# Performance work log

Hardware: AMD Instinct MI355X
Metric: run time of the kernel (lower is better)

The kernel has to match this reference:

```python
import jax, jax.numpy as jnp
import numpy as np

D_MODEL, D_STATE, D_CONV, EXPAND = 1024, 16, 4, 2
D_INNER = EXPAND * D_MODEL            # 2048
DT_RANK = (D_MODEL + 15) // 16        # 64
B, L = 2, 2048


def setup_inputs() -> dict:
    key = jax.random.key(0)
    ks = jax.random.split(key, 10)
    s = 0.02
    x = jax.random.normal(ks[0], (B, L, D_MODEL), dtype=jnp.float32)
    W_in = jax.random.normal(ks[1], (2 * D_INNER, D_MODEL), dtype=jnp.float32) * s
    conv_w = jax.random.normal(ks[2], (D_INNER, D_CONV), dtype=jnp.float32) * s
    conv_b = jnp.zeros((D_INNER,), dtype=jnp.float32)
    W_xproj = jax.random.normal(ks[3], (DT_RANK + 2 * D_STATE, D_INNER), dtype=jnp.float32) * s
    W_dtproj = jax.random.normal(ks[4], (D_INNER, DT_RANK), dtype=jnp.float32) * s
    dt_bias = jax.random.uniform(ks[5], (D_INNER,), dtype=jnp.float32, minval=-4.0, maxval=-2.0)
    # S4D-real init: A_log = log(1..d_state) per channel
    A_log = jnp.log(jnp.broadcast_to(jnp.arange(1, D_STATE + 1, dtype=jnp.float32), (D_INNER, D_STATE)))
    D = jnp.ones((D_INNER,), dtype=jnp.float32)
    W_out = jax.random.normal(ks[6], (D_MODEL, D_INNER), dtype=jnp.float32) * s
    return dict(x=x, W_in=W_in, conv_w=conv_w, conv_b=conv_b, W_xproj=W_xproj,
                W_dtproj=W_dtproj, dt_bias=dt_bias, A_log=A_log, D=D, W_out=W_out)


def _mamba_forward(x, W_in, conv_w, conv_b, W_xproj, W_dtproj, dt_bias, A_log, D, W_out):
    # in_proj: (B,L,d_model) -> (B,L,2*d_inner)
    xz = jnp.einsum('bld,ed->ble', x, W_in)
    u, z = jnp.split(xz, 2, axis=-1)                      # (B,L,Di) each
    # depthwise causal conv over time
    u_t = jnp.swapaxes(u, 1, 2)                           # (B,Di,L)
    u_c = jax.lax.conv_general_dilated(
        u_t, conv_w[:, None, :], window_strides=(1,), padding=[(D_CONV - 1, 0)],
        feature_group_count=D_INNER, dimension_numbers=('NCH', 'OIH', 'NCH'))
    u_c = jax.nn.silu(u_c + conv_b[None, :, None])
    u_c = jnp.swapaxes(u_c, 1, 2)                         # (B,L,Di)
    # x_proj -> dt, B_ssm, C_ssm
    x_dbl = jnp.einsum('bld,ed->ble', u_c, W_xproj)
    dt, B_ssm, C_ssm = jnp.split(x_dbl, [DT_RANK, DT_RANK + D_STATE], axis=-1)
    delta = jax.nn.softplus(jnp.einsum('blr,dr->bld', dt, W_dtproj) + dt_bias)  # (B,L,Di)
    A = -jnp.exp(A_log)                                   # (Di,Ds)

    def step(h, inp):
        d_t, b_t, c_t, u_t = inp                          # (B,Di),(B,Ds),(B,Ds),(B,Di)
        dA = jnp.exp(d_t[..., None] * A)                  # (B,Di,Ds)
        dBu = d_t[..., None] * b_t[:, None, :] * u_t[..., None]
        h = dA * h + dBu
        y = jnp.einsum('bds,bs->bd', h, c_t)
        return h, y

    h0 = jnp.zeros((B, D_INNER, D_STATE), dtype=x.dtype)
    xs = (jnp.swapaxes(delta, 0, 1), jnp.swapaxes(B_ssm, 0, 1),
          jnp.swapaxes(C_ssm, 0, 1), jnp.swapaxes(u_c, 0, 1))
    _, ys = jax.lax.scan(step, h0, xs)                    # (L,B,Di)
    y = jnp.swapaxes(ys, 0, 1) + u_c * D                  # skip term D*u
    y = y * jax.nn.silu(z)                                # gate
    return jnp.einsum('bld,ed->ble', y, W_out)            # (B,L,d_model)


def reference(x, W_in, conv_w, conv_b, W_xproj, W_dtproj, dt_bias, A_log, D, W_out):
    return _mamba_forward(x, W_in, conv_w, conv_b, W_xproj, W_dtproj, dt_bias, A_log, D, W_out)
```

## Files before the change

### kernel.cpp

```cpp
#include <hip/hip_runtime.h>
#include <cstdint>
#include <cstddef>

constexpr int Bc = 2, Lc = 2048, DM = 1024, DI = 2048, DS = 16, DR = 64, NX = 96;
constexpr int BL = Bc * Lc;
constexpr int NC = 32, CH = 64;
constexpr int BDS = Bc * DI * DS;
constexpr float LOG2E = 1.44269504f;

typedef __attribute__((ext_vector_type(8))) short bf16x8;
typedef __attribute__((ext_vector_type(4))) float f32x4;
typedef unsigned short u16;

__device__ __forceinline__ u16 f2b(float f) {
  uint32_t u = __float_as_uint(f);
  return (u16)((u + 0x7FFFu + ((u >> 16) & 1u)) >> 16);
}
__device__ __forceinline__ float b2f(u16 h) {
  return __uint_as_float(((uint32_t)h) << 16);
}

__global__ __launch_bounds__(256) void cvt_hilo(
    const float* __restrict__ in, u16* __restrict__ hi, u16* __restrict__ lo,
    int n4) {
  int i = blockIdx.x * 256 + threadIdx.x;
  if (i >= n4) return;
  float4 v = reinterpret_cast<const float4*>(in)[i];
  ushort4 H, L;
  H.x = f2b(v.x); L.x = f2b(v.x - b2f(H.x));
  H.y = f2b(v.y); L.y = f2b(v.y - b2f(H.y));
  H.z = f2b(v.z); L.z = f2b(v.z - b2f(H.z));
  H.w = f2b(v.w); L.w = f2b(v.w - b2f(H.w));
  reinterpret_cast<ushort4*>(hi)[i] = H;
  reinterpret_cast<ushort4*>(lo)[i] = L;
}

__global__ __launch_bounds__(256) void cvt_pad_wx(
    const float* __restrict__ w, u16* __restrict__ hi, u16* __restrict__ lo) {
  int i = blockIdx.x * 256 + threadIdx.x;
  int f = i * 4;
  int row = f >> 11;
  ushort4 H, L;
  H.x = H.y = H.z = H.w = 0; L = H;
  if (row < 96) {
    float4 v = *reinterpret_cast<const float4*>(&w[f]);
    H.x = f2b(v.x); L.x = f2b(v.x - b2f(H.x));
    H.y = f2b(v.y); L.y = f2b(v.y - b2f(H.y));
    H.z = f2b(v.z); L.z = f2b(v.z - b2f(H.z));
    H.w = f2b(v.w); L.w = f2b(v.w - b2f(H.w));
  }
  reinterpret_cast<ushort4*>(hi)[i] = H;
  reinterpret_cast<ushort4*>(lo)[i] = L;
}

__device__ __forceinline__ void stage_tile(
    const u16* __restrict__ g, u16* lds, int row0, int ld, int k0,
    int w, int lane) {
  #pragma unroll
  for (int i = 0; i < 2; ++i) {
    const int base = w * 1024 + i * 4096;
    const int o = base + lane * 16;
    const int row = o >> 6;
    const int sl = ((o >> 4) & 3) ^ ((row >> 1) & 3);
    const u16* src = g + (size_t)(row0 + row) * ld + (k0 + sl * 8);
    __builtin_amdgcn_global_load_lds(
        (const __attribute__((address_space(1))) unsigned int*)src,
        (__attribute__((address_space(3))) unsigned int*)(lds + base / 2),
        16, 0, 0);
  }
}

__device__ __forceinline__ void stage4(
    const u16* __restrict__ Ah, const u16* __restrict__ Al,
    const u16* __restrict__ Bh, const u16* __restrict__ Bl,
    u16* buf , int bm, int bn, int lda, int ldb,
    int k0, int w, int lane) {
  stage_tile(Ah, buf + 0 * 4096, bm, lda, k0, w, lane);
  stage_tile(Al, buf + 1 * 4096, bm, lda, k0, w, lane);
  stage_tile(Bh, buf + 2 * 4096, bn, ldb, k0, w, lane);
  stage_tile(Bl, buf + 3 * 4096, bn, ldb, k0, w, lane);
}

__device__ __forceinline__ bf16x8 ld_frag(const u16* plane, int rowbase, int lane) {
  const int row = rowbase + (lane & 15);
  const int kb = (lane >> 4) ^ ((row >> 1) & 3);
  return *reinterpret_cast<const bf16x8*>(
      reinterpret_cast<const char*>(plane) + row * 64 + kb * 16);
}

template<int EPI>
__global__ __launch_bounds__(256) void gemm_mfma(
    const u16* __restrict__ Ah, const u16* __restrict__ Al,
    const u16* __restrict__ Bh, const u16* __restrict__ Bl,
    const float* __restrict__ bias, float* __restrict__ C,
    int M, int N, int K, int lda, int ldb, int ldc) {
  __shared__ __align__(16) u16 lds[2][4][4096];
  const int tid = threadIdx.x;
  const int lane = tid & 63, w = tid >> 6;
  const int wr = w >> 1, wc = w & 1;
  const int bm = blockIdx.x * 128, bn = blockIdx.y * 128;

  f32x4 acc[4][4] = {};

  const int nt = K / 32;
  stage4(Ah, Al, Bh, Bl, &lds[0][0][0], bm, bn, lda, ldb, 0, w, lane);
  __syncthreads();

  int cur = 0;
  for (int t = 0; t < nt; ++t) {
    if (t + 1 < nt)
      stage4(Ah, Al, Bh, Bl, &lds[cur ^ 1][0][0], bm, bn, lda, ldb,
             (t + 1) * 32, w, lane);

    const u16* Lb = &lds[cur][0][0];
    bf16x8 ah[4], al[4], bh[4], bl[4];
    #pragma unroll
    for (int m = 0; m < 4; ++m) {
      ah[m] = ld_frag(Lb + 0 * 4096, wr * 64 + m * 16, lane);
      al[m] = ld_frag(Lb + 1 * 4096, wr * 64 + m * 16, lane);
    }
    #pragma unroll
    for (int n = 0; n < 4; ++n) {
      bh[n] = ld_frag(Lb + 2 * 4096, wc * 64 + n * 16, lane);
      bl[n] = ld_frag(Lb + 3 * 4096, wc * 64 + n * 16, lane);
    }
    __builtin_amdgcn_s_setprio(1);
    #pragma unroll
    for (int m = 0; m < 4; ++m)
      #pragma unroll
      for (int n = 0; n < 4; ++n)
        acc[m][n] = __builtin_amdgcn_mfma_f32_16x16x32_bf16(ah[m], bh[n], acc[m][n], 0, 0, 0);
    #pragma unroll
    for (int m = 0; m < 4; ++m)
      #pragma unroll
      for (int n = 0; n < 4; ++n)
        acc[m][n] = __builtin_amdgcn_mfma_f32_16x16x32_bf16(ah[m], bl[n], acc[m][n], 0, 0, 0);
    #pragma unroll
    for (int m = 0; m < 4; ++m)
      #pragma unroll
      for (int n = 0; n < 4; ++n)
        acc[m][n] = __builtin_amdgcn_mfma_f32_16x16x32_bf16(al[m], bh[n], acc[m][n], 0, 0, 0);
    __builtin_amdgcn_s_setprio(0);
    __syncthreads();
    cur ^= 1;
  }

  const int rbase = (lane >> 4) * 4;
  const int cidx = lane & 15;
  #pragma unroll
  for (int m = 0; m < 4; ++m) {
    int grow0 = bm + wr * 64 + m * 16 + rbase;
    #pragma unroll
    for (int n = 0; n < 4; ++n) {
      int gcol = bn + wc * 64 + n * 16 + cidx;
      if (gcol < N) {
        #pragma unroll
        for (int r = 0; r < 4; ++r) {
          float v = acc[m][n][r];
          if (EPI == 1) {
            v += bias[gcol];
            v = fmaxf(v, 0.f) + log1pf(expf(-fabsf(v)));
          }
          C[(size_t)(grow0 + r) * ldc + gcol] = v;
        }
      }
    }
  }
}

__global__ __launch_bounds__(256) void conv_silu(
    const float* __restrict__ xz, const float* __restrict__ w,
    const float* __restrict__ bias, u16* __restrict__ uch,
    u16* __restrict__ ucl) {
  int idx = blockIdx.x * blockDim.x + threadIdx.x;
  int d  = idx & (DI - 1);
  int bl = idx >> 11;
  int b  = bl >> 11;
  int l  = bl & (Lc - 1);
  float4 wv = *reinterpret_cast<const float4*>(&w[d * 4]);
  float acc = bias[d];
  const float wk[4] = {wv.x, wv.y, wv.z, wv.w};
  #pragma unroll
  for (int k = 0; k < 4; ++k) {
    int ls = l - 3 + k;
    if (ls >= 0) acc = fmaf(xz[((size_t)(b * Lc + ls)) * (2 * DI) + d], wk[k], acc);
  }
  acc = acc * __frcp_rn(1.f + __expf(-acc));
  u16 h = f2b(acc);
  uch[idx] = h;
  ucl[idx] = f2b(acc - b2f(h));
}

__global__ __launch_bounds__(256) void scan_chunk_local(
    const float* __restrict__ delta, const u16* __restrict__ uch,
    const u16* __restrict__ ucl, const float* __restrict__ xdbl,
    const float* __restrict__ A_log, float* __restrict__ Pa,
    float* __restrict__ hA) {
  const int t = blockIdx.x * 256 + threadIdx.x;
  const int d = t & (DI - 1);
  const int b = (t >> 11) & (Bc - 1);
  const int c = t >> 12;
  const int bd = (b << 11) | d;

  float Av2[DS];
  {
    const float4* ap = reinterpret_cast<const float4*>(&A_log[(size_t)d * DS]);
    #pragma unroll
    for (int q = 0; q < 4; ++q) {
      float4 a = ap[q];
      Av2[4*q+0] = -LOG2E * __expf(a.x);
      Av2[4*q+1] = -LOG2E * __expf(a.y);
      Av2[4*q+2] = -LOG2E * __expf(a.z);
      Av2[4*q+3] = -LOG2E * __expf(a.w);
    }
  }
  const size_t rowbase = (size_t)(b * Lc + c * CH);
  const float* dp  = delta + rowbase * DI + d;
  const u16*   uhp = uch   + rowbase * DI + d;
  const u16*   ulp = ucl   + rowbase * DI + d;
  const float4* xp = reinterpret_cast<const float4*>(xdbl + rowbase * NX + DR);

  float h[DS] = {};
  float S = 0.f;
  float dt = dp[0];
  float ut = b2f(uhp[0]) + b2f(ulp[0]);
  float4 B0 = xp[0], B1 = xp[1], B2 = xp[2], B3 = xp[3];

  for (int l = 0; l < CH; ++l) {
    const int ln = (l + 1 < CH) ? l + 1 : l;
    float dtn = dp[ln * DI];
    float utn = b2f(uhp[ln * DI]) + b2f(ulp[ln * DI]);
    const float4* xn = xp + ln * (NX / 4);
    float4 B0n = xn[0], B1n = xn[1], B2n = xn[2], B3n = xn[3];

    float Bs[16];
    *reinterpret_cast<float4*>(&Bs[0])  = B0;
    *reinterpret_cast<float4*>(&Bs[4])  = B1;
    *reinterpret_cast<float4*>(&Bs[8])  = B2;
    *reinterpret_cast<float4*>(&Bs[12]) = B3;
    const float dtu = dt * ut;
    S += dt;
    #pragma unroll
    for (int s = 0; s < DS; ++s) {
      float dA = exp2f(dt * Av2[s]);
      h[s] = fmaf(dA, h[s], dtu * Bs[s]);
    }
    dt = dtn; ut = utn; B0 = B0n; B1 = B1n; B2 = B2n; B3 = B3n;
  }

  float4* Pp = reinterpret_cast<float4*>(&Pa[(size_t)c * BDS + (size_t)bd * DS]);
  float4* Hp = reinterpret_cast<float4*>(&hA[(size_t)c * BDS + (size_t)bd * DS]);
  #pragma unroll
  for (int q = 0; q < 4; ++q) {
    float4 pv, hv;
    pv.x = exp2f(Av2[4*q+0] * S); pv.y = exp2f(Av2[4*q+1] * S);
    pv.z = exp2f(Av2[4*q+2] * S); pv.w = exp2f(Av2[4*q+3] * S);
    hv.x = h[4*q+0]; hv.y = h[4*q+1]; hv.z = h[4*q+2]; hv.w = h[4*q+3];
    Pp[q] = pv; Hp[q] = hv;
  }
}

__global__ __launch_bounds__(256) void scan_chunk_carry(
    float* Pa_h0, const float* __restrict__ hA) {
  const int t = blockIdx.x * 256 + threadIdx.x;
  float pa[NC], ha[NC];
  #pragma unroll
  for (int c = 0; c < NC; ++c) {
    pa[c] = Pa_h0[(size_t)c * BDS + t];
    ha[c] = hA[(size_t)c * BDS + t];
  }
  float h = 0.f;
  #pragma unroll
  for (int c = 0; c < NC; ++c) {
    Pa_h0[(size_t)c * BDS + t] = h;
    h = fmaf(pa[c], h, ha[c]);
  }
}

__global__ __launch_bounds__(256) void scan_chunk_final(
    const float* __restrict__ delta, const u16* uch, const u16* ucl,
    const float* __restrict__ xdbl, const float* __restrict__ xz,
    const float* __restrict__ A_log, const float* __restrict__ Dv,
    const float* __restrict__ h0, u16* yh, u16* yl) {
  const int t = blockIdx.x * 256 + threadIdx.x;
  const int d = t & (DI - 1);
  const int b = (t >> 11) & (Bc - 1);
  const int c = t >> 12;
  const int bd = (b << 11) | d;

  float Av2[DS];
  {
    const float4* ap = reinterpret_cast<const float4*>(&A_log[(size_t)d * DS]);
    #pragma unroll
    for (int q = 0; q < 4; ++q) {
      float4 a = ap[q];
      Av2[4*q+0] = -LOG2E * __expf(a.x);
      Av2[4*q+1] = -LOG2E * __expf(a.y);
      Av2[4*q+2] = -LOG2E * __expf(a.z);
      Av2[4*q+3] = -LOG2E * __expf(a.w);
    }
  }
  const float Dd = Dv[d];
  float h[DS];
  {
    const float4* hp = reinterpret_cast<const float4*>(&h0[(size_t)c * BDS + (size_t)bd * DS]);
    #pragma unroll
    for (int q = 0; q < 4; ++q) {
      float4 hv = hp[q];
      h[4*q+0] = hv.x; h[4*q+1] = hv.y; h[4*q+2] = hv.z; h[4*q+3] = hv.w;
    }
  }
  const size_t rowbase = (size_t)(b * Lc + c * CH);
  const float* dp  = delta + rowbase * DI + d;
  const u16*   uhp = uch   + rowbase * DI + d;
  const u16*   ulp = ucl   + rowbase * DI + d;
  const float* zp  = xz    + rowbase * (2 * DI) + DI + d;
  const float4* xp = reinterpret_cast<const float4*>(xdbl + rowbase * NX + DR);
  u16* yhp = yh + rowbase * DI + d;
  u16* ylp = yl + rowbase * DI + d;

  float dt = dp[0];
  float ut = b2f(uhp[0]) + b2f(ulp[0]);
  float zt = zp[0];
  float4 B0 = xp[0], B1 = xp[1], B2 = xp[2], B3 = xp[3];
  float4 C0 = xp[4], C1 = xp[5], C2 = xp[6], C3 = xp[7];

  for (int l = 0; l < CH; ++l) {
    const int ln = (l + 1 < CH) ? l + 1 : l;
    float dtn = dp[ln * DI];
    float utn = b2f(uhp[ln * DI]) + b2f(ulp[ln * DI]);
    float ztn = zp[ln * (2 * DI)];
    const float4* xn = xp + ln * (NX / 4);
    float4 B0n = xn[0], B1n = xn[1], B2n = xn[2], B3n = xn[3];
    float4 C0n = xn[4], C1n = xn[5], C2n = xn[6], C3n = xn[7];

    float Bs[16], Cs[16];
    *reinterpret_cast<float4*>(&Bs[0])  = B0;
    *reinterpret_cast<float4*>(&Bs[4])  = B1;
    *reinterpret_cast<float4*>(&Bs[8])  = B2;
    *reinterpret_cast<float4*>(&Bs[12]) = B3;
    *reinterpret_cast<float4*>(&Cs[0])  = C0;
    *reinterpret_cast<float4*>(&Cs[4])  = C1;
    *reinterpret_cast<float4*>(&Cs[8])  = C2;
    *reinterpret_cast<float4*>(&Cs[12]) = C3;
    const float dtu = dt * ut;
    float y0 = 0.f, y1 = 0.f;
    #pragma unroll
    for (int s = 0; s < DS; ++s) {
      float dA = exp2f(dt * Av2[s]);
      h[s] = fmaf(dA, h[s], dtu * Bs[s]);
      if (s & 1) y1 = fmaf(h[s], Cs[s], y1);
      else       y0 = fmaf(h[s], Cs[s], y0);
    }
    float gate = zt * __frcp_rn(1.f + exp2f(-LOG2E * zt));
    float y = (y0 + y1 + Dd * ut) * gate;
    u16 hh = f2b(y);
    yhp[l * DI] = hh;
    ylp[l * DI] = f2b(y - b2f(hh));

    dt = dtn; ut = utn; zt = ztn;
    B0 = B0n; B1 = B1n; B2 = B2n; B3 = B3n;
    C0 = C0n; C1 = C1n; C2 = C2n; C3 = C3n;
  }
}

extern "C" void kernel_launch(void* const* d_in, const int* in_sizes, int n_in,
                              void* d_out, int out_size, void* d_ws, size_t ws_size,
                              hipStream_t stream) {
  const float* x        = (const float*)d_in[0];
  const float* W_in     = (const float*)d_in[1];
  const float* conv_w   = (const float*)d_in[2];
  const float* conv_b   = (const float*)d_in[3];
  const float* W_xproj  = (const float*)d_in[4];
  const float* W_dtproj = (const float*)d_in[5];
  const float* dt_bias  = (const float*)d_in[6];
  const float* A_log    = (const float*)d_in[7];
  const float* Dv       = (const float*)d_in[8];
  const float* W_out    = (const float*)d_in[9];
  float* out = (float*)d_out;

  char* W = (char*)d_ws;
  size_t off = 0;
  float* xz  = (float*)(W + off);  off += (size_t)BL * 4096 * 4;
  size_t delta_off = off;
  u16* xh   = (u16*)(W + off);     off += (size_t)BL * DM * 2;
  u16* xl   = (u16*)(W + off);     off += (size_t)BL * DM * 2;
  u16* Wih  = (u16*)(W + off);     off += (size_t)(2 * DI) * DM * 2;
  u16* Wil  = (u16*)(W + off);     off += (size_t)(2 * DI) * DM * 2;
  float* delta = (float*)(W + delta_off);
  u16* uch  = (u16*)(W + off);     off += (size_t)BL * DI * 2;
  u16* ucl  = (u16*)(W + off);     off += (size_t)BL * DI * 2;
  u16* Wxh  = (u16*)(W + off);     off += (size_t)128 * DI * 2;
  u16* Wxl  = (u16*)(W + off);     off += (size_t)128 * DI * 2;
  float* xdbl = (float*)(W + off); off += (size_t)BL * NX * 4;
  u16* xdh  = (u16*)(W + off);     off += (size_t)BL * NX * 2;
  u16* xdl  = (u16*)(W + off);     off += (size_t)BL * NX * 2;
  u16* Wdh  = (u16*)(W + off);     off += (size_t)DI * DR * 2;
  u16* Wdl  = (u16*)(W + off);     off += (size_t)DI * DR * 2;
  u16* Woh  = (u16*)(W + off);     off += (size_t)DM * DI * 2;
  u16* Wol  = (u16*)(W + off);     off += (size_t)DM * DI * 2;
  float* Pa = (float*)(W + off);   off += (size_t)NC * BDS * 4;
  float* hA = (float*)(W + off);   off += (size_t)NC * BDS * 4;
  float* h0 = Pa;
  u16* yh = uch;
  u16* yl = ucl;

  cvt_hilo<<<(BL * DM / 4 + 255) / 256, 256, 0, stream>>>(x, xh, xl, BL * DM / 4);
  cvt_hilo<<<(2 * DI * DM / 4 + 255) / 256, 256, 0, stream>>>(W_in, Wih, Wil, 2 * DI * DM / 4);
  cvt_pad_wx<<<(128 * DI / 4) / 256, 256, 0, stream>>>(W_xproj, Wxh, Wxl);
  cvt_hilo<<<(DI * DR / 4 + 255) / 256, 256, 0, stream>>>(W_dtproj, Wdh, Wdl, DI * DR / 4);
  cvt_hilo<<<(DM * DI / 4 + 255) / 256, 256, 0, stream>>>(W_out, Woh, Wol, DM * DI / 4);

  gemm_mfma<0><<<dim3(BL / 128, (2 * DI) / 128), 256, 0, stream>>>(
      xh, xl, Wih, Wil, nullptr, xz, BL, 2 * DI, DM, DM, DM, 2 * DI);

  conv_silu<<<(BL * DI) / 256, 256, 0, stream>>>(xz, conv_w, conv_b, uch, ucl);

  gemm_mfma<0><<<dim3(BL / 128, 1), 256, 0, stream>>>(
      uch, ucl, Wxh, Wxl, nullptr, xdbl, BL, NX, DI, DI, DI, NX);

  cvt_hilo<<<(BL * NX / 4 + 255) / 256, 256, 0, stream>>>(xdbl, xdh, xdl, BL * NX / 4);

  gemm_mfma<1><<<dim3(BL / 128, DI / 128), 256, 0, stream>>>(
      xdh, xdl, Wdh, Wdl, dt_bias, delta, BL, DI, DR, NX, DR, DI);

  scan_chunk_local<<<(Bc * DI * NC) / 256, 256, 0, stream>>>(
      delta, uch, ucl, xdbl, A_log, Pa, hA);
  scan_chunk_carry<<<BDS / 256, 256, 0, stream>>>(Pa, hA);
  scan_chunk_final<<<(Bc * DI * NC) / 256, 256, 0, stream>>>(
      delta, uch, ucl, xdbl, xz, A_log, Dv, h0, yh, yl);

  gemm_mfma<0><<<dim3(BL / 128, DM / 128), 256, 0, stream>>>(
      yh, yl, Woh, Wol, nullptr, out, BL, DM, DI, DI, DI, DM);
}
```

Measured before the change: 468.8 us.

## Retile bf16x3 GEMM to 8 waves with K=64, split-K x_proj, vectorize conv

The shared split-bf16 MFMA GEMM now runs with 512 threads (8 waves) and a 64-wide K stage. The LDS swizzle is widened to match, and each wave holds a 32x64 sub-tile. The skinny x_proj GEMM (N=96) is split 8 ways along K into a partial buffer that aliases the scan scratch. A new reduce kernel sums the partials and also produces the hi/lo bf16 split, replacing the separate cvt_hilo launch. The depthwise conv+SiLU kernel handles four channels per thread with float4 loads, at the cost of more LDS per block (128KB) and extra partial-sum traffic.

Measured after the change: 437.6 us. 1.07x faster.

```diff
diff --git a/kernel.cpp b/kernel.cpp
--- a/kernel.cpp
+++ b/kernel.cpp
@@ -6,6 +6,7 @@
 constexpr int BL = Bc * Lc;
 constexpr int NC = 32, CH = 64;
 constexpr int BDS = Bc * DI * DS;
+constexpr int NSK = 8;
 constexpr float LOG2E = 1.44269504f;
 
 typedef __attribute__((ext_vector_type(8))) short bf16x8;
@@ -58,10 +59,10 @@
     int w, int lane) {
   #pragma unroll
   for (int i = 0; i < 2; ++i) {
-    const int base = w * 1024 + i * 4096;
+    const int base = w * 1024 + i * 8192;
     const int o = base + lane * 16;
-    const int row = o >> 6;
-    const int sl = ((o >> 4) & 3) ^ ((row >> 1) & 3);
+    const int row = o >> 7;
+    const int sl = ((o >> 4) & 7) ^ (row & 7);
     const u16* src = g + (size_t)(row0 + row) * ld + (k0 + sl * 8);
     __builtin_amdgcn_global_load_lds(
         (const __attribute__((address_space(1))) unsigned int*)src,
@@ -75,34 +76,40 @@
     const u16* __restrict__ Bh, const u16* __restrict__ Bl,
     u16* buf , int bm, int bn, int lda, int ldb,
     int k0, int w, int lane) {
-  stage_tile(Ah, buf + 0 * 4096, bm, lda, k0, w, lane);
-  stage_tile(Al, buf + 1 * 4096, bm, lda, k0, w, lane);
-  stage_tile(Bh, buf + 2 * 4096, bn, ldb, k0, w, lane);
-  stage_tile(Bl, buf + 3 * 4096, bn, ldb, k0, w, lane);
-}
-
-__device__ __forceinline__ bf16x8 ld_frag(const u16* plane, int rowbase, int lane) {
+  stage_tile(Ah, buf + 0 * 8192, bm, lda, k0, w, lane);
+  stage_tile(Al, buf + 1 * 8192, bm, lda, k0, w, lane);
+  stage_tile(Bh, buf + 2 * 8192, bn, ldb, k0, w, lane);
+  stage_tile(Bl, buf + 3 * 8192, bn, ldb, k0, w, lane);
+}
+
+__device__ __forceinline__ bf16x8 ld_frag(const u16* plane, int rowbase,
+                                          int kk, int lane) {
   const int row = rowbase + (lane & 15);
-  const int kb = (lane >> 4) ^ ((row >> 1) & 3);
+  const int kb = ((kk << 2) | (lane >> 4)) ^ (row & 7);
   return *reinterpret_cast<const bf16x8*>(
-      reinterpret_cast<const char*>(plane) + row * 64 + kb * 16);
+      reinterpret_cast<const char*>(plane) + row * 128 + kb * 16);
 }
 
 template<int EPI>
-__global__ __launch_bounds__(256) void gemm_mfma(
+__global__ __launch_bounds__(512) void gemm_mfma(
     const u16* __restrict__ Ah, const u16* __restrict__ Al,
     const u16* __restrict__ Bh, const u16* __restrict__ Bl,
     const float* __restrict__ bias, float* __restrict__ C,
-    int M, int N, int K, int lda, int ldb, int ldc) {
-  __shared__ __align__(16) u16 lds[2][4][4096];
+    int M, int N, int kEff, int lda, int ldb, int ldc,
+    size_t cSplitStride) {
+  __shared__ __align__(16) u16 lds[2][4][8192];
   const int tid = threadIdx.x;
   const int lane = tid & 63, w = tid >> 6;
   const int wr = w >> 1, wc = w & 1;
   const int bm = blockIdx.x * 128, bn = blockIdx.y * 128;
-
-  f32x4 acc[4][4] = {};
-
-  const int nt = K / 32;
+  const int sk = blockIdx.z;
+  Ah += (size_t)sk * kEff; Al += (size_t)sk * kEff;
+  Bh += (size_t)sk * kEff; Bl += (size_t)sk * kEff;
+  C  += (size_t)sk * cSplitStride;
+
+  f32x4 acc[2][4] = {};
+  const int nt = kEff >> 6;
+
   stage4(Ah, Al, Bh, Bl, &lds[0][0][0], bm, bn, lda, ldb, 0, w, lane);
   __syncthreads();
 
@@ -110,37 +117,40 @@
   for (int t = 0; t < nt; ++t) {
     if (t + 1 < nt)
       stage4(Ah, Al, Bh, Bl, &lds[cur ^ 1][0][0], bm, bn, lda, ldb,
-             (t + 1) * 32, w, lane);
+             (t + 1) * 64, w, lane);
 
     const u16* Lb = &lds[cur][0][0];
-    bf16x8 ah[4], al[4], bh[4], bl[4];
-    #pragma unroll
-    for (int m = 0; m < 4; ++m) {
-      ah[m] = ld_frag(Lb + 0 * 4096, wr * 64 + m * 16, lane);
-      al[m] = ld_frag(Lb + 1 * 4096, wr * 64 + m * 16, lane);
-    }
-    #pragma unroll
-    for (int n = 0; n < 4; ++n) {
-      bh[n] = ld_frag(Lb + 2 * 4096, wc * 64 + n * 16, lane);
-      bl[n] = ld_frag(Lb + 3 * 4096, wc * 64 + n * 16, lane);
-    }
-    __builtin_amdgcn_s_setprio(1);
-    #pragma unroll
-    for (int m = 0; m < 4; ++m)
+    #pragma unroll
+    for (int kk = 0; kk < 2; ++kk) {
+      bf16x8 ah[2], al[2], bh[4], bl[4];
       #pragma unroll
-      for (int n = 0; n < 4; ++n)
-        acc[m][n] = __builtin_amdgcn_mfma_f32_16x16x32_bf16(ah[m], bh[n], acc[m][n], 0, 0, 0);
-    #pragma unroll
-    for (int m = 0; m < 4; ++m)
+      for (int m = 0; m < 2; ++m) {
+        ah[m] = ld_frag(Lb + 0 * 8192, wr * 32 + m * 16, kk, lane);
+        al[m] = ld_frag(Lb + 1 * 8192, wr * 32 + m * 16, kk, lane);
+      }
       #pragma unroll
-      for (int n = 0; n < 4; ++n)
-        acc[m][n] = __builtin_amdgcn_mfma_f32_16x16x32_bf16(ah[m], bl[n], acc[m][n], 0, 0, 0);
-    #pragma unroll
-    for (int m = 0; m < 4; ++m)
+      for (int n = 0; n < 4; ++n) {
+        bh[n] = ld_frag(Lb + 2 * 8192, wc * 64 + n * 16, kk, lane);
+        bl[n] = ld_frag(Lb + 3 * 8192, wc * 64 + n * 16, kk, lane);
+      }
+      __builtin_amdgcn_s_setprio(1);
       #pragma unroll
-      for (int n = 0; n < 4; ++n)
-        acc[m][n] = __builtin_amdgcn_mfma_f32_16x16x32_bf16(al[m], bh[n], acc[m][n], 0, 0, 0);
-    __builtin_amdgcn_s_setprio(0);
+      for (int m = 0; m < 2; ++m)
+        #pragma unroll
+        for (int n = 0; n < 4; ++n)
+          acc[m][n] = __builtin_amdgcn_mfma_f32_16x16x32_bf16(ah[m], bh[n], acc[m][n], 0, 0, 0);
+      #pragma unroll
+      for (int m = 0; m < 2; ++m)
+        #pragma unroll
+        for (int n = 0; n < 4; ++n)
+          acc[m][n] = __builtin_amdgcn_mfma_f32_16x16x32_bf16(ah[m], bl[n], acc[m][n], 0, 0, 0);
+      #pragma unroll
+      for (int m = 0; m < 2; ++m)
+        #pragma unroll
+        for (int n = 0; n < 4; ++n)
+          acc[m][n] = __builtin_amdgcn_mfma_f32_16x16x32_bf16(al[m], bh[n], acc[m][n], 0, 0, 0);
+      __builtin_amdgcn_s_setprio(0);
+    }
     __syncthreads();
     cur ^= 1;
   }
@@ -148,8 +158,8 @@
   const int rbase = (lane >> 4) * 4;
   const int cidx = lane & 15;
   #pragma unroll
-  for (int m = 0; m < 4; ++m) {
-    int grow0 = bm + wr * 64 + m * 16 + rbase;
+  for (int m = 0; m < 2; ++m) {
+    int grow0 = bm + wr * 32 + m * 16 + rbase;
     #pragma unroll
     for (int n = 0; n < 4; ++n) {
       int gcol = bn + wc * 64 + n * 16 + cidx;
@@ -168,27 +178,62 @@
   }
 }
 
-__global__ __launch_bounds__(256) void conv_silu(
+__global__ __launch_bounds__(256) void xproj_reduce(
+    const float* __restrict__ pbuf, float* __restrict__ xdbl,
+    u16* __restrict__ xdh, u16* __restrict__ xdl) {
+  int i = blockIdx.x * 256 + threadIdx.x;
+  const float4* p = reinterpret_cast<const float4*>(pbuf);
+  float4 s = p[i];
+  #pragma unroll
+  for (int sk = 1; sk < NSK; ++sk) {
+    float4 v = p[(size_t)sk * (BL * NX / 4) + i];
+    s.x += v.x; s.y += v.y; s.z += v.z; s.w += v.w;
+  }
+  reinterpret_cast<float4*>(xdbl)[i] = s;
+  ushort4 H, L;
+  H.x = f2b(s.x); L.x = f2b(s.x - b2f(H.x));
+  H.y = f2b(s.y); L.y = f2b(s.y - b2f(H.y));
+  H.z = f2b(s.z); L.z = f2b(s.z - b2f(H.z));
+  H.w = f2b(s.w); L.w = f2b(s.w - b2f(H.w));
+  reinterpret_cast<ushort4*>(xdh)[i] = H;
+  reinterpret_cast<ushort4*>(xdl)[i] = L;
+}
+
+__global__ __launch_bounds__(256) void conv_silu4(
     const float* __restrict__ xz, const float* __restrict__ w,
     const float* __restrict__ bias, u16* __restrict__ uch,
     u16* __restrict__ ucl) {
-  int idx = blockIdx.x * blockDim.x + threadIdx.x;
-  int d  = idx & (DI - 1);
-  int bl = idx >> 11;
+  int i = blockIdx.x * 256 + threadIdx.x;
+  int d4 = (i << 2) & (DI - 1);
+  int bl = i >> 9;
   int b  = bl >> 11;
   int l  = bl & (Lc - 1);
-  float4 wv = *reinterpret_cast<const float4*>(&w[d * 4]);
-  float acc = bias[d];
-  const float wk[4] = {wv.x, wv.y, wv.z, wv.w};
+  const float4* wrow = reinterpret_cast<const float4*>(&w[d4 * 4]);
+  float4 w0 = wrow[0], w1 = wrow[1], w2 = wrow[2], w3 = wrow[3];
+  float4 a = *reinterpret_cast<const float4*>(&bias[d4]);
   #pragma unroll
   for (int k = 0; k < 4; ++k) {
     int ls = l - 3 + k;
-    if (ls >= 0) acc = fmaf(xz[((size_t)(b * Lc + ls)) * (2 * DI) + d], wk[k], acc);
-  }
-  acc = acc * __frcp_rn(1.f + __expf(-acc));
-  u16 h = f2b(acc);
-  uch[idx] = h;
-  ucl[idx] = f2b(acc - b2f(h));
+    if (ls >= 0) {
+      float4 xv = *reinterpret_cast<const float4*>(
+          &xz[((size_t)(b * Lc + ls)) * (2 * DI) + d4]);
+      a.x = fmaf(xv.x, (&w0.x)[k], a.x);
+      a.y = fmaf(xv.y, (&w1.x)[k], a.y);
+      a.z = fmaf(xv.z, (&w2.x)[k], a.z);
+      a.w = fmaf(xv.w, (&w3.x)[k], a.w);
+    }
+  }
+  a.x = a.x * __frcp_rn(1.f + __expf(-a.x));
+  a.y = a.y * __frcp_rn(1.f + __expf(-a.y));
+  a.z = a.z * __frcp_rn(1.f + __expf(-a.z));
+  a.w = a.w * __frcp_rn(1.f + __expf(-a.w));
+  ushort4 H, L;
+  H.x = f2b(a.x); L.x = f2b(a.x - b2f(H.x));
+  H.y = f2b(a.y); L.y = f2b(a.y - b2f(H.y));
+  H.z = f2b(a.z); L.z = f2b(a.z - b2f(H.z));
+  H.w = f2b(a.w); L.w = f2b(a.w - b2f(H.w));
+  reinterpret_cast<ushort4*>(uch)[i] = H;
+  reinterpret_cast<ushort4*>(ucl)[i] = L;
 }
 
 __global__ __launch_bounds__(256) void scan_chunk_local(
@@ -402,6 +447,7 @@
   float* Pa = (float*)(W + off);   off += (size_t)NC * BDS * 4;
   float* hA = (float*)(W + off);   off += (size_t)NC * BDS * 4;
   float* h0 = Pa;
+  float* pbuf = Pa;
   u16* yh = uch;
   u16* yl = ucl;
 
@@ -411,18 +457,19 @@
   cvt_hilo<<<(DI * DR / 4 + 255) / 256, 256, 0, stream>>>(W_dtproj, Wdh, Wdl, DI * DR / 4);
   cvt_hilo<<<(DM * DI / 4 + 255) / 256, 256, 0, stream>>>(W_out, Woh, Wol, DM * DI / 4);
 
-  gemm_mfma<0><<<dim3(BL / 128, (2 * DI) / 128), 256, 0, stream>>>(
-      xh, xl, Wih, Wil, nullptr, xz, BL, 2 * DI, DM, DM, DM, 2 * DI);
-
-  conv_silu<<<(BL * DI) / 256, 256, 0, stream>>>(xz, conv_w, conv_b, uch, ucl);
-
-  gemm_mfma<0><<<dim3(BL / 128, 1), 256, 0, stream>>>(
-      uch, ucl, Wxh, Wxl, nullptr, xdbl, BL, NX, DI, DI, DI, NX);
-
-  cvt_hilo<<<(BL * NX / 4 + 255) / 256, 256, 0, stream>>>(xdbl, xdh, xdl, BL * NX / 4);
-
-  gemm_mfma<1><<<dim3(BL / 128, DI / 128), 256, 0, stream>>>(
-      xdh, xdl, Wdh, Wdl, dt_bias, delta, BL, DI, DR, NX, DR, DI);
+  gemm_mfma<0><<<dim3(BL / 128, (2 * DI) / 128, 1), 512, 0, stream>>>(
+      xh, xl, Wih, Wil, nullptr, xz, BL, 2 * DI, DM, DM, DM, 2 * DI, 0);
+
+  conv_silu4<<<(BL * DI / 4) / 256, 256, 0, stream>>>(xz, conv_w, conv_b, uch, ucl);
+
+  gemm_mfma<0><<<dim3(BL / 128, 1, NSK), 512, 0, stream>>>(
+      uch, ucl, Wxh, Wxl, nullptr, pbuf, BL, NX, DI / NSK, DI, DI, NX,
+      (size_t)BL * NX);
+
+  xproj_reduce<<<(BL * NX / 4) / 256, 256, 0, stream>>>(pbuf, xdbl, xdh, xdl);
+
+  gemm_mfma<1><<<dim3(BL / 128, DI / 128, 1), 512, 0, stream>>>(
+      xdh, xdl, Wdh, Wdl, dt_bias, delta, BL, DI, DR, NX, DR, DI, 0);
 
   scan_chunk_local<<<(Bc * DI * NC) / 256, 256, 0, stream>>>(
       delta, uch, ucl, xdbl, A_log, Pa, hA);
@@ -430,6 +477,6 @@
   scan_chunk_final<<<(Bc * DI * NC) / 256, 256, 0, stream>>>(
       delta, uch, ucl, xdbl, xz, A_log, Dv, h0, yh, yl);
 
-  gemm_mfma<0><<<dim3(BL / 128, DM / 128), 256, 0, stream>>>(
-      yh, yl, Woh, Wol, nullptr, out, BL, DM, DI, DI, DI, DM);
-}
+  gemm_mfma<0><<<dim3(BL / 128, DM / 128, 1), 512, 0, stream>>>(
+      yh, yl, Woh, Wol, nullptr, out, BL, DM, DI, DI, DI, DM, 0);
+}
```
